# Performance work log

Hardware: AMD Instinct MI355X
Metric: run time of the kernel (lower is better)

Reference implementation:

```python
import jax, jax.numpy as jnp
import numpy as np

N = 50000      # nodes
E = 600000     # edges
D = 128        # embedding_dim
H = 256        # GENConv MLP hidden = 2*D (expansion=2, num_layers=2)
L = 2          # n_layers
EPS_MSG = 1e-7
EPS_NORM = 1e-5


def setup_inputs() -> dict:
    key = jax.random.key(0)
    ks = jax.random.split(key, 16)
    s = 0.05
    inp = {}
    inp["x"] = jax.random.normal(ks[0], (N, 1), jnp.float32)
    inp["edge_index"] = jax.random.randint(ks[1], (2, E), 0, N)
    inp["edge_attr"] = jax.random.normal(ks[2], (E, 1), jnp.float32)
    # encoders
    inp["Wn"] = jax.random.normal(ks[3], (1, D), jnp.float32) * s
    inp["bn_b"] = jnp.zeros((D,), jnp.float32)
    inp["We"] = jax.random.normal(ks[4], (1, D), jnp.float32) * s
    inp["be"] = jnp.zeros((D,), jnp.float32)
    # per-layer BatchNorm affine
    inp["bn_gamma"] = jnp.ones((L, D), jnp.float32)
    inp["bn_beta"] = jnp.zeros((L, D), jnp.float32)
    # per-layer GENConv params: learnable temperature t, MLP [D->H->D] with LayerNorm
    inp["t"] = jnp.ones((L,), jnp.float32)
    inp["W1"] = jax.random.normal(ks[5], (L, D, H), jnp.float32) * s
    inp["b1"] = jnp.zeros((L, H), jnp.float32)
    inp["ln_g"] = jnp.ones((L, H), jnp.float32)
    inp["ln_b"] = jnp.zeros((L, H), jnp.float32)
    inp["W2"] = jax.random.normal(ks[6], (L, H, D), jnp.float32) * s
    inp["b2"] = jnp.zeros((L, D), jnp.float32)
    return inp


def _segment_softmax(logits, seg, num):
    # per-channel softmax over edges grouped by destination node
    m = jax.ops.segment_max(logits, seg, num_segments=num)
    m = jnp.where(jnp.isfinite(m), m, 0.0)  # empty segments
    ex = jnp.exp(logits - m[seg])
    den = jax.ops.segment_sum(ex, seg, num_segments=num)
    return ex / (den[seg] + 1e-16)


def reference(x, edge_index, edge_attr, Wn, bn_b, We, be,
              bn_gamma, bn_beta, t, W1, b1, ln_g, ln_b, W2, b2):
    src, dst = edge_index[0], edge_index[1]
    h = x @ Wn + bn_b                 # [N, D] node encoder
    e = edge_attr @ We + be           # [E, D] edge encoder
    for l in range(L):
        # DeepGCNLayer 'res+': h_in -> BN -> ReLU -> conv -> + h_in
        mu = h.mean(axis=0)
        var = h.var(axis=0)
        hn = (h - mu) / jnp.sqrt(var + EPS_NORM) * bn_gamma[l] + bn_beta[l]
        hn = jax.nn.relu(hn)
        # GENConv: msg = relu(x_j + e) + eps; softmax-aggr with temperature t
        msg = jax.nn.relu(hn[src] + e) + EPS_MSG          # [E, D]
        alpha = _segment_softmax(msg * t[l], dst, N)      # [E, D]
        agg = jax.ops.segment_sum(msg * alpha, dst, num_segments=N)  # [N, D]
        out = agg + hn                                    # add root
        # GENConv MLP: Linear -> LayerNorm -> ReLU -> Linear
        z = out @ W1[l] + b1[l]
        zm = z.mean(axis=-1, keepdims=True)
        zv = z.var(axis=-1, keepdims=True)
        z = (z - zm) / jnp.sqrt(zv + EPS_NORM) * ln_g[l] + ln_b[l]
        z = jax.nn.relu(z)
        z = z @ W2[l] + b2[l]
        h = h + z                                         # res+ residual
    # DotProductPredictor over the same edge list
    return (h[src] * h[dst]).sum(axis=-1)                 # [E]
```

## Files before the change

kernel.cpp:

```cpp
#include <hip/hip_runtime.h>
#include <hip/hip_bf16.h>
#include <math.h>

#define NN 50000
#define NE 600000
#define MPAD 50048
#define DIM 128
#define HID 256
#define NB 49
#define HIST_BLOCKS ((NE + 255) / 256)
#define CAST_BLOCKS ((4 * DIM * HID) / 256)
#define EPS_MSG 1e-7f
#define EPS_NORM 1e-5f

typedef __attribute__((ext_vector_type(8))) short short8v;
typedef __attribute__((ext_vector_type(8))) unsigned short ushort8v;
typedef __attribute__((ext_vector_type(4))) float f32x4;

__device__ inline ushort f2bf(float f) {
    union { float f; unsigned u; } v; v.f = f;
    unsigned r = v.u + 0x7FFF + ((v.u >> 16) & 1);
    return (ushort)(r >> 16);
}
__device__ inline float bf2f(ushort u) {
    union { unsigned u; float f; } v; v.u = (unsigned)u << 16; return v.f;
}

__global__ __launch_bounds__(256) void k_setup(const float* __restrict__ x,
                                               const int* __restrict__ dst,
                                               const float* __restrict__ W1,
                                               const float* __restrict__ W2,
                                               float* __restrict__ xs,
                                               int* __restrict__ deg,
                                               ushort* __restrict__ W1t,
                                               ushort* __restrict__ W2t) {
    int b = blockIdx.x;
    if (b < 64) {
        int lane = threadIdx.x & 63;
        float s = 0.f, q = 0.f;
        for (int i = b * 256 + threadIdx.x; i < NN; i += 64 * 256) {
            float v = x[i];
            s += v; q += v * v;
        }
        #pragma unroll
        for (int off = 32; off >= 1; off >>= 1) {
            s += __shfl_xor(s, off, 64);
            q += __shfl_xor(q, off, 64);
        }
        if (lane == 0) { atomicAdd(&xs[0], s); atomicAdd(&xs[1], q); }
    } else if (b < 64 + HIST_BLOCKS) {
        int i = (b - 64) * 256 + threadIdx.x;
        if (i < NE) atomicAdd(&deg[dst[i]], 1);
    } else {
        const int chunk = DIM * HID;
        int i = (b - 64 - HIST_BLOCKS) * 256 + threadIdx.x;
        int w = i / chunk;
        int j = i - w * chunk;
        if (w < 2) {
            int r = j / HID, c = j - r * HID;
            W1t[(size_t)w * chunk + (size_t)c * DIM + r] = f2bf(W1[(size_t)w * chunk + j]);
        } else {
            int l = w - 2;
            int r = j / DIM, c = j - r * DIM;
            W2t[(size_t)l * chunk + (size_t)c * HID + r] = f2bf(W2[(size_t)l * chunk + j]);
        }
    }
}

__global__ void k_hn0(const float* __restrict__ x, const float* __restrict__ xs,
                      const float* __restrict__ Wn, const float* __restrict__ bnb,
                      const float* __restrict__ gamma, const float* __restrict__ beta,
                      ushort* __restrict__ hn, int total4) {
    int i = blockIdx.x * blockDim.x + threadIdx.x;
    if (i >= total4) return;
    int d4 = (i & 31) * 4;
    int n = i >> 5;
    float mx = xs[0] * (1.f / NN);
    float vx = xs[1] * (1.f / NN) - mx * mx;
    float xv = x[n];
    float4 w = *(const float4*)(Wn + d4);
    float4 b = *(const float4*)(bnb + d4);
    float4 g = *(const float4*)(gamma + d4);
    float4 bt = *(const float4*)(beta + d4);
    ushort4 o;
    {
        float mu = fmaf(mx, w.x, b.x), sc = rsqrtf(vx * w.x * w.x + EPS_NORM) * g.x;
        o.x = f2bf(fmaxf(fmaf(fmaf(xv, w.x, b.x) - mu, sc, bt.x), 0.f));
    }
    {
        float mu = fmaf(mx, w.y, b.y), sc = rsqrtf(vx * w.y * w.y + EPS_NORM) * g.y;
        o.y = f2bf(fmaxf(fmaf(fmaf(xv, w.y, b.y) - mu, sc, bt.y), 0.f));
    }
    {
        float mu = fmaf(mx, w.z, b.z), sc = rsqrtf(vx * w.z * w.z + EPS_NORM) * g.z;
        o.z = f2bf(fmaxf(fmaf(fmaf(xv, w.z, b.z) - mu, sc, bt.z), 0.f));
    }
    {
        float mu = fmaf(mx, w.w, b.w), sc = rsqrtf(vx * w.w * w.w + EPS_NORM) * g.w;
        o.w = f2bf(fmaxf(fmaf(fmaf(xv, w.w, b.w) - mu, sc, bt.w), 0.f));
    }
    *(ushort4*)(hn + (size_t)n * DIM + d4) = o;
}

__global__ __launch_bounds__(256) void k_scanA(const int* __restrict__ deg,
                                               int* __restrict__ partials, int n) {
    __shared__ int ws[4];
    int b = blockIdx.x;
    int t = threadIdx.x;
    int s = 0;
    #pragma unroll
    for (int i = 0; i < 4; ++i) {
        int idx = b * 1024 + t + i * 256;
        s += (idx < n) ? deg[idx] : 0;
    }
    #pragma unroll
    for (int off = 32; off >= 1; off >>= 1) s += __shfl_xor(s, off, 64);
    if ((t & 63) == 0) ws[t >> 6] = s;
    __syncthreads();
    if (t == 0) partials[b] = ws[0] + ws[1] + ws[2] + ws[3];
}

__global__ __launch_bounds__(64) void k_scanB(const int* __restrict__ partials,
                                              int* __restrict__ base,
                                              int* __restrict__ row_off) {
    int t = threadIdx.x;
    int v = (t < NB) ? partials[t] : 0;
    int x = v;
    #pragma unroll
    for (int off = 1; off < 64; off <<= 1) {
        int y = __shfl_up(x, off, 64);
        if (t >= off) x += y;
    }
    if (t < NB) base[t] = x - v;
    if (t == 0) row_off[NN] = NE;
}

__global__ __launch_bounds__(1024) void k_scanC(const int* __restrict__ deg,
                                                const int* __restrict__ base,
                                                int* __restrict__ row_off,
                                                int* __restrict__ cursor, int n) {
    __shared__ int wsum[16];
    int i = blockIdx.x * 1024 + threadIdx.x;
    int lane = threadIdx.x & 63;
    int wid = threadIdx.x >> 6;
    int v = (i < n) ? deg[i] : 0;
    int x = v;
    #pragma unroll
    for (int off = 1; off < 64; off <<= 1) {
        int y = __shfl_up(x, off, 64);
        if (lane >= off) x += y;
    }
    if (lane == 63) wsum[wid] = x;
    __syncthreads();
    if (wid == 0 && lane < 16) {
        int w = wsum[lane];
        #pragma unroll
        for (int off = 1; off < 16; off <<= 1) {
            int y = __shfl_up(w, off, 64);
            if (lane >= off) w += y;
        }
        wsum[lane] = w;
    }
    __syncthreads();
    int prev = (wid == 0) ? 0 : wsum[wid - 1];
    int excl = base[blockIdx.x] + prev + (x - v);
    if (i < n) { row_off[i] = excl; cursor[i] = excl; }
}

__global__ void k_scatter(const int* __restrict__ src, const int* __restrict__ dst,
                          const float* __restrict__ eattr, int* __restrict__ cursor,
                          int4* __restrict__ erec, int E) {
    int i = blockIdx.x * blockDim.x + threadIdx.x;
    if (i >= E) return;
    int d = dst[i];
    int pos = atomicAdd(&cursor[d], 1);
    erec[pos] = make_int4(src[i], i, __float_as_int(eattr[i]), 0);
}

__global__ void k_bn_relu(const float* __restrict__ h, const float* __restrict__ stats,
                          const float* __restrict__ gamma, const float* __restrict__ beta,
                          ushort* __restrict__ hn, int total4) {
    int i = blockIdx.x * blockDim.x + threadIdx.x;
    if (i >= total4) return;
    int d4 = (i & 31) * 4;
    int n = i >> 5;
    float4 v = *(const float4*)(h + (size_t)n * DIM + d4);
    float4 s = *(const float4*)(stats + d4);
    float4 q = *(const float4*)(stats + DIM + d4);
    float4 g = *(const float4*)(gamma + d4);
    float4 bt = *(const float4*)(beta + d4);
    ushort4 o;
    {
        float mu = s.x * (1.f / NN), var = q.x * (1.f / NN) - mu * mu;
        float sc = rsqrtf(var + EPS_NORM) * g.x;
        o.x = f2bf(fmaxf(fmaf(v.x - mu, sc, bt.x), 0.f));
    }
    {
        float mu = s.y * (1.f / NN), var = q.y * (1.f / NN) - mu * mu;
        float sc = rsqrtf(var + EPS_NORM) * g.y;
        o.y = f2bf(fmaxf(fmaf(v.y - mu, sc, bt.y), 0.f));
    }
    {
        float mu = s.z * (1.f / NN), var = q.z * (1.f / NN) - mu * mu;
        float sc = rsqrtf(var + EPS_NORM) * g.z;
        o.z = f2bf(fmaxf(fmaf(v.z - mu, sc, bt.z), 0.f));
    }
    {
        float mu = s.w * (1.f / NN), var = q.w * (1.f / NN) - mu * mu;
        float sc = rsqrtf(var + EPS_NORM) * g.w;
        o.w = f2bf(fmaxf(fmaf(v.w - mu, sc, bt.w), 0.f));
    }
    *(ushort4*)(hn + (size_t)n * DIM + d4) = o;
}

__global__ __launch_bounds__(256) void k_agg(const ushort* __restrict__ hn,
                                             const int4* __restrict__ erec,
                                             const int* __restrict__ row_off,
                                             const float* __restrict__ We,
                                             const float* __restrict__ be,
                                             const float* __restrict__ t_all, int l,
                                             ushort* __restrict__ ob, int N) {
    int n = blockIdx.x * 4 + (threadIdx.x >> 6);
    if (n >= N) return;
    int lane = threadIdx.x & 63;
    int d0 = lane * 2;
    float2 we = *(const float2*)(We + d0);
    float2 bd = *(const float2*)(be + d0);
    float t = t_all[l];
    int p0 = row_off[n], p1 = row_off[n + 1];
    int deg = p1 - p0;

    int mp = p0 + lane;
    int s_l = 0; float ea_l = 0.f;
    if (mp < p1) {
        int4 r = erec[mp];
        s_l = r.x; ea_l = __int_as_float(r.z);
    }

    float den0 = 0.f, num0 = 0.f, den1 = 0.f, num1 = 0.f;
    int kmax = deg < 64 ? deg : 64;
    int k = 0;
    for (; k + 4 <= kmax; k += 4) {
        int sA = __shfl(s_l, k, 64), sB = __shfl(s_l, k + 1, 64);
        int sC = __shfl(s_l, k + 2, 64), sD = __shfl(s_l, k + 3, 64);
        float eA = __shfl(ea_l, k, 64), eB = __shfl(ea_l, k + 1, 64);
        float eC = __shfl(ea_l, k + 2, 64), eD = __shfl(ea_l, k + 3, 64);
        uint hA = *(const uint*)(hn + (size_t)sA * DIM + d0);
        uint hB = *(const uint*)(hn + (size_t)sB * DIM + d0);
        uint hC = *(const uint*)(hn + (size_t)sC * DIM + d0);
        uint hD = *(const uint*)(hn + (size_t)sD * DIM + d0);
        {
            float m0 = fmaxf(bf2f((ushort)hA) + fmaf(eA, we.x, bd.x), 0.f) + EPS_MSG;
            float m1 = fmaxf(bf2f((ushort)(hA >> 16)) + fmaf(eA, we.y, bd.y), 0.f) + EPS_MSG;
            float x0 = __expf(m0 * t), x1 = __expf(m1 * t);
            den0 += x0; num0 += m0 * x0; den1 += x1; num1 += m1 * x1;
        }
        {
            float m0 = fmaxf(bf2f((ushort)hB) + fmaf(eB, we.x, bd.x), 0.f) + EPS_MSG;
            float m1 = fmaxf(bf2f((ushort)(hB >> 16)) + fmaf(eB, we.y, bd.y), 0.f) + EPS_MSG;
            float x0 = __expf(m0 * t), x1 = __expf(m1 * t);
            den0 += x0; num0 += m0 * x0; den1 += x1; num1 += m1 * x1;
        }
        {
            float m0 = fmaxf(bf2f((ushort)hC) + fmaf(eC, we.x, bd.x), 0.f) + EPS_MSG;
            float m1 = fmaxf(bf2f((ushort)(hC >> 16)) + fmaf(eC, we.y, bd.y), 0.f) + EPS_MSG;
            float x0 = __expf(m0 * t), x1 = __expf(m1 * t);
            den0 += x0; num0 += m0 * x0; den1 += x1; num1 += m1 * x1;
        }
        {
            float m0 = fmaxf(bf2f((ushort)hD) + fmaf(eD, we.x, bd.x), 0.f) + EPS_MSG;
            float m1 = fmaxf(bf2f((ushort)(hD >> 16)) + fmaf(eD, we.y, bd.y), 0.f) + EPS_MSG;
            float x0 = __expf(m0 * t), x1 = __expf(m1 * t);
            den0 += x0; num0 += m0 * x0; den1 += x1; num1 += m1 * x1;
        }
    }
    for (; k < kmax; ++k) {
        int s = __shfl(s_l, k, 64);
        float ea = __shfl(ea_l, k, 64);
        uint hv = *(const uint*)(hn + (size_t)s * DIM + d0);
        float m0 = fmaxf(bf2f((ushort)hv) + fmaf(ea, we.x, bd.x), 0.f) + EPS_MSG;
        float m1 = fmaxf(bf2f((ushort)(hv >> 16)) + fmaf(ea, we.y, bd.y), 0.f) + EPS_MSG;
        float x0 = __expf(m0 * t), x1 = __expf(m1 * t);
        den0 += x0; num0 += m0 * x0; den1 += x1; num1 += m1 * x1;
    }
    for (int p = p0 + 64; p < p1; ++p) {
        int4 r = erec[p];
        int s = r.x;
        float ea = __int_as_float(r.z);
        uint hv = *(const uint*)(hn + (size_t)s * DIM + d0);
        float m0 = fmaxf(bf2f((ushort)hv) + fmaf(ea, we.x, bd.x), 0.f) + EPS_MSG;
        float m1 = fmaxf(bf2f((ushort)(hv >> 16)) + fmaf(ea, we.y, bd.y), 0.f) + EPS_MSG;
        float x0 = __expf(m0 * t), x1 = __expf(m1 * t);
        den0 += x0; num0 += m0 * x0; den1 += x1; num1 += m1 * x1;
    }
    uint hr = *(const uint*)(hn + (size_t)n * DIM + d0);
    float a0 = (deg > 0) ? num0 / (den0 + 1e-16f) : 0.f;
    float a1 = (deg > 0) ? num1 / (den1 + 1e-16f) : 0.f;
    uint o = (uint)f2bf(a0 + bf2f((ushort)hr)) |
             ((uint)f2bf(a1 + bf2f((ushort)(hr >> 16))) << 16);
    *(uint*)(ob + (size_t)n * DIM + d0) = o;
}

template <int FIRST>
__global__ __launch_bounds__(256) void k_mlp(const ushort* __restrict__ A,
                                             const ushort* __restrict__ B1t,
                                             const float* __restrict__ b1,
                                             const float* __restrict__ g,
                                             const float* __restrict__ bv,
                                             const ushort* __restrict__ B2t,
                                             const float* __restrict__ b2,
                                             const float* __restrict__ x,
                                             const float* __restrict__ Wn,
                                             const float* __restrict__ bnb,
                                             float* __restrict__ C,
                                             ushort* __restrict__ hb,
                                             float* __restrict__ stats) {
    constexpr int LDZ = 264;
    __shared__ ushort Zs[32 * LDZ];
    __shared__ float red_s[4][32];
    __shared__ float red_q[4][32];
    __shared__ float murs[2][32];
    const int tid = threadIdx.x;
    const int lane = tid & 63;
    const int wid = tid >> 6;
    const int row0 = blockIdx.x * 32;
    const int wc = wid * 64;
    const int l15 = lane & 15;
    const int lq = lane >> 4;

    f32x4 acc[2][4] = {};
    #pragma unroll
    for (int ks = 0; ks < 4; ++ks) {
        int kk = ks * 32 + lq * 8;
        short8v bfr[4], afr[2];
        #pragma unroll
        for (int f = 0; f < 4; ++f)
            bfr[f] = *(const short8v*)(B1t + (size_t)(wc + f * 16 + l15) * DIM + kk);
        #pragma unroll
        for (int f = 0; f < 2; ++f)
            afr[f] = *(const short8v*)(A + (size_t)(row0 + f * 16 + l15) * DIM + kk);
        #pragma unroll
        for (int mi = 0; mi < 2; ++mi)
            #pragma unroll
            for (int ni = 0; ni < 4; ++ni)
                acc[mi][ni] = __builtin_amdgcn_mfma_f32_16x16x32_bf16(
                    afr[mi], bfr[ni], acc[mi][ni], 0, 0, 0);
    }

    float bb[4], gg[4], bb2[4];
    #pragma unroll
    for (int ni = 0; ni < 4; ++ni) {
        int col = wc + ni * 16 + l15;
        bb[ni] = b1[col]; gg[ni] = g[col]; bb2[ni] = bv[col];
    }
    #pragma unroll
    for (int mi = 0; mi < 2; ++mi) {
        #pragma unroll
        for (int j = 0; j < 4; ++j) {
            float s = 0.f, q = 0.f;
            #pragma unroll
            for (int ni = 0; ni < 4; ++ni) {
                float v = acc[mi][ni][j] + bb[ni];
                acc[mi][ni][j] = v;
                s += v; q += v * v;
            }
            #pragma unroll
            for (int off = 1; off <= 8; off <<= 1) {
                s += __shfl_xor(s, off, 64);
                q += __shfl_xor(q, off, 64);
            }
            if (l15 == 0) {
                int row = mi * 16 + lq * 4 + j;
                red_s[wid][row] = s;
                red_q[wid][row] = q;
            }
        }
    }
    __syncthreads();
    if (tid < 32) {
        float s = red_s[0][tid] + red_s[1][tid] + red_s[2][tid] + red_s[3][tid];
        float q = red_q[0][tid] + red_q[1][tid] + red_q[2][tid] + red_q[3][tid];
        float mu = s * (1.f / HID);
        float var = q * (1.f / HID) - mu * mu;
        murs[0][tid] = mu;
        murs[1][tid] = rsqrtf(var + EPS_NORM);
    }
    __syncthreads();
    #pragma unroll
    for (int mi = 0; mi < 2; ++mi) {
        #pragma unroll
        for (int j = 0; j < 4; ++j) {
            int row = mi * 16 + lq * 4 + j;
            float mu = murs[0][row], rs = murs[1][row];
            #pragma unroll
            for (int ni = 0; ni < 4; ++ni) {
                float v = fmaxf(fmaf((acc[mi][ni][j] - mu) * rs, gg[ni], bb2[ni]), 0.f);
                Zs[row * LDZ + wc + ni * 16 + l15] = f2bf(v);
            }
        }
    }
    __syncthreads();

    const int wc2 = wid * 32;
    f32x4 acc2[2][2] = {};
    #pragma unroll
    for (int ks = 0; ks < 8; ++ks) {
        int kk = ks * 32 + lq * 8;
        short8v bf2[2], af2[2];
        #pragma unroll
        for (int f = 0; f < 2; ++f)
            bf2[f] = *(const short8v*)(B2t + (size_t)(wc2 + f * 16 + l15) * HID + kk);
        #pragma unroll
        for (int f = 0; f < 2; ++f)
            af2[f] = *(const short8v*)(Zs + (f * 16 + l15) * LDZ + kk);
        #pragma unroll
        for (int mi = 0; mi < 2; ++mi)
            #pragma unroll
            for (int ni = 0; ni < 2; ++ni)
                acc2[mi][ni] = __builtin_amdgcn_mfma_f32_16x16x32_bf16(
                    af2[mi], bf2[ni], acc2[mi][ni], 0, 0, 0);
    }

    float ssum[2] = {0.f, 0.f};
    float sq[2] = {0.f, 0.f};
    #pragma unroll
    for (int ni = 0; ni < 2; ++ni) {
        int col = wc2 + ni * 16 + l15;
        float bvv = b2[col];
        float wnc = FIRST ? Wn[col] : 0.f;
        float bnc = FIRST ? bnb[col] : 0.f;
        #pragma unroll
        for (int mi = 0; mi < 2; ++mi) {
            int rowb = row0 + mi * 16 + lq * 4;
            #pragma unroll
            for (int j = 0; j < 4; ++j) {
                int gr = rowb + j;
                float base;
                if (FIRST) {
                    float xv = (gr < NN) ? x[gr] : 0.f;
                    base = fmaf(xv, wnc, bnc);
                } else {
                    base = C[(size_t)gr * DIM + col];
                }
                float v = acc2[mi][ni][j] + bvv + base;
                if (FIRST) {
                    C[(size_t)gr * DIM + col] = v;
                    bool ok = gr < NN;
                    ssum[ni] += ok ? v : 0.f;
                    sq[ni] += ok ? v * v : 0.f;
                } else {
                    hb[(size_t)gr * DIM + col] = f2bf(v);
                }
            }
        }
    }
    if (FIRST) {
        #pragma unroll
        for (int ni = 0; ni < 2; ++ni) {
            float s = ssum[ni], q = sq[ni];
            s += __shfl_xor(s, 16, 64); s += __shfl_xor(s, 32, 64);
            q += __shfl_xor(q, 16, 64); q += __shfl_xor(q, 32, 64);
            if (lq == 0) {
                int col = wc2 + ni * 16 + l15;
                atomicAdd(&stats[col], s);
                atomicAdd(&stats[DIM + col], q);
            }
        }
    }
}

__global__ __launch_bounds__(256) void k_dot(const ushort* __restrict__ hb,
                                             const int4* __restrict__ erec,
                                             const int* __restrict__ row_off,
                                             float* __restrict__ out, int N) {
    int n = blockIdx.x * 4 + (threadIdx.x >> 6);
    if (n >= N) return;
    int lane = threadIdx.x & 63;
    int sub = lane >> 4;
    int l16 = lane & 15;
    float hd[8];
    {
        ushort8v hv = *(const ushort8v*)(hb + (size_t)n * DIM + l16 * 8);
        #pragma unroll
        for (int j = 0; j < 8; ++j) hd[j] = bf2f(hv[j]);
    }
    int p0 = row_off[n], p1 = row_off[n + 1];
    int deg = p1 - p0;
    int mp = p0 + lane;
    int s_l = 0, e_l = 0;
    if (mp < p1) {
        int4 r = erec[mp];
        s_l = r.x; e_l = r.y;
    }
    int kmax = deg < 64 ? deg : 64;
    for (int k = 0; k < kmax; k += 4) {
        int idx = k + sub;
        bool ok = idx < kmax;
        int s = __shfl(s_l, idx, 64);
        int e = __shfl(e_l, idx, 64);
        ushort8v av = *(const ushort8v*)(hb + (size_t)(ok ? s : n) * DIM + l16 * 8);
        float p = 0.f;
        #pragma unroll
        for (int j = 0; j < 8; ++j) p = fmaf(bf2f(av[j]), hd[j], p);
        p += __shfl_xor(p, 1, 16);
        p += __shfl_xor(p, 2, 16);
        p += __shfl_xor(p, 4, 16);
        p += __shfl_xor(p, 8, 16);
        if (ok && l16 == 0) out[e] = p;
    }
    for (int pb = p0 + 64; pb < p1; pb += 4) {
        int pe = pb + sub;
        bool ok = pe < p1;
        int s = n, e = 0;
        if (ok) { int4 r = erec[pe]; s = r.x; e = r.y; }
        ushort8v av = *(const ushort8v*)(hb + (size_t)s * DIM + l16 * 8);
        float p = 0.f;
        #pragma unroll
        for (int j = 0; j < 8; ++j) p = fmaf(bf2f(av[j]), hd[j], p);
        p += __shfl_xor(p, 1, 16);
        p += __shfl_xor(p, 2, 16);
        p += __shfl_xor(p, 4, 16);
        p += __shfl_xor(p, 8, 16);
        if (ok && l16 == 0) out[e] = p;
    }
}

extern "C" void kernel_launch(void* const* d_in, const int* in_sizes, int n_in,
                              void* d_out, int out_size, void* d_ws, size_t ws_size,
                              hipStream_t stream) {
    const float* x        = (const float*)d_in[0];
    const int*   ei       = (const int*)d_in[1];
    const float* eattr    = (const float*)d_in[2];
    const float* Wn       = (const float*)d_in[3];
    const float* bnb      = (const float*)d_in[4];
    const float* We       = (const float*)d_in[5];
    const float* be       = (const float*)d_in[6];
    const float* bn_gamma = (const float*)d_in[7];
    const float* bn_beta  = (const float*)d_in[8];
    const float* t_all    = (const float*)d_in[9];
    const float* W1       = (const float*)d_in[10];
    const float* b1       = (const float*)d_in[11];
    const float* ln_g     = (const float*)d_in[12];
    const float* ln_b     = (const float*)d_in[13];
    const float* W2       = (const float*)d_in[14];
    const float* b2       = (const float*)d_in[15];
    float* out = (float*)d_out;

    const int N = NN, E = NE, D = DIM, H = HID;
    const int* src = ei;
    const int* dst = ei + E;

    char* ws = (char*)d_ws;
    auto alloc = [&](size_t bytes) {
        char* p = ws;
        ws += (bytes + 255) & ~(size_t)255;
        return p;
    };
    float*  h       = (float*)alloc((size_t)MPAD * D * 4);
    ushort* ob      = (ushort*)alloc((size_t)MPAD * D * 2);
    ushort* hn      = (ushort*)alloc((size_t)MPAD * D * 2);
    ushort* hb      = (ushort*)alloc((size_t)MPAD * D * 2);
    ushort* W1t     = (ushort*)alloc((size_t)2 * D * H * 2);
    ushort* W2t     = (ushort*)alloc((size_t)2 * D * H * 2);
    int4*   erec    = (int4*)alloc((size_t)E * 16);
    int*    row_off = (int*)alloc((size_t)(N + 1) * 4);
    int*    cursor  = (int*)alloc((size_t)N * 4);
    int*    deg     = (int*)alloc((size_t)N * 4);
    int*    partials= (int*)alloc((size_t)64 * 4);
    int*    pbase   = (int*)alloc((size_t)64 * 4);
    float*  stats   = (float*)alloc((size_t)2 * D * 4);
    float*  xs      = (float*)alloc((size_t)2 * 4);

    hipMemsetAsync(deg, 0, (size_t)N * 4, stream);
    hipMemsetAsync(stats, 0, 1024 + 8, stream);

    k_setup<<<64 + HIST_BLOCKS + CAST_BLOCKS, 256, 0, stream>>>(x, dst, W1, W2,
                                                                xs, deg, W1t, W2t);
    k_scanA<<<NB, 256, 0, stream>>>(deg, partials, N);
    k_scanB<<<1, 64, 0, stream>>>(partials, pbase, row_off);
    k_scanC<<<NB, 1024, 0, stream>>>(deg, pbase, row_off, cursor, N);
    k_scatter<<<(E + 255) / 256, 256, 0, stream>>>(src, dst, eattr, cursor, erec, E);
    k_hn0<<<(N * 32 + 255) / 256, 256, 0, stream>>>(x, xs, Wn, bnb, bn_gamma, bn_beta,
                                                    hn, N * 32);

    k_agg<<<(N + 3) / 4, 256, 0, stream>>>(hn, erec, row_off, We, be, t_all, 0, ob, N);
    k_mlp<1><<<MPAD / 32, 256, 0, stream>>>(ob, W1t, b1, ln_g, ln_b, W2t, b2,
                                            x, Wn, bnb, h, hb, stats);
    k_bn_relu<<<(N * 32 + 255) / 256, 256, 0, stream>>>(h, stats, bn_gamma + D, bn_beta + D,
                                                        hn, N * 32);

    k_agg<<<(N + 3) / 4, 256, 0, stream>>>(hn, erec, row_off, We, be, t_all, 1, ob, N);
    k_mlp<0><<<MPAD / 32, 256, 0, stream>>>(ob, W1t + (size_t)D * H, b1 + H,
                                            ln_g + H, ln_b + H, W2t + (size_t)D * H, b2 + D,
                                            x, Wn, bnb, h, hb, stats);

    k_dot<<<(N + 3) / 4, 256, 0, stream>>>(hb, erec, row_off, out, N);
}
```

Measured before the change: 384.0 us.

## Make MLP kernel persistent with register-resident weight fragments

The fused MLP kernel becomes persistent: a fixed grid of 512 blocks loops over 32-row tiles. Each wave loads its W1 and W2 fragments into registers once and reuses them across tiles, instead of reloading them from global memory for every tile. The A tile is loaded fully before the MFMA loop, and launch bounds request two blocks per CU. This removes repeated weight traffic but raises register pressure, about 48 short8 weight vectors per thread, which may cause spills or lower occupancy.

```diff
diff --git a/kernel.cpp b/kernel.cpp
--- a/kernel.cpp
+++ b/kernel.cpp
@@ -5,6 +5,7 @@
 #define NN 50000
 #define NE 600000
 #define MPAD 50048
+#define NT (MPAD / 32)
 #define DIM 128
 #define HID 256
 #define NB 49
@@ -302,19 +303,19 @@
 }
 
 template <int FIRST>
-__global__ __launch_bounds__(256) void k_mlp(const ushort* __restrict__ A,
-                                             const ushort* __restrict__ B1t,
-                                             const float* __restrict__ b1,
-                                             const float* __restrict__ g,
-                                             const float* __restrict__ bv,
-                                             const ushort* __restrict__ B2t,
-                                             const float* __restrict__ b2,
-                                             const float* __restrict__ x,
-                                             const float* __restrict__ Wn,
-                                             const float* __restrict__ bnb,
-                                             float* __restrict__ C,
-                                             ushort* __restrict__ hb,
-                                             float* __restrict__ stats) {
+__global__ __launch_bounds__(256, 2) void k_mlp(const ushort* __restrict__ A,
+                                                const ushort* __restrict__ B1t,
+                                                const float* __restrict__ b1,
+                                                const float* __restrict__ g,
+                                                const float* __restrict__ bv,
+                                                const ushort* __restrict__ B2t,
+                                                const float* __restrict__ b2,
+                                                const float* __restrict__ x,
+                                                const float* __restrict__ Wn,
+                                                const float* __restrict__ bnb,
+                                                float* __restrict__ C,
+                                                ushort* __restrict__ hb,
+                                                float* __restrict__ stats) {
     constexpr int LDZ = 264;
     __shared__ ushort Zs[32 * LDZ];
     __shared__ float red_s[4][32];
@@ -323,149 +324,166 @@
     const int tid = threadIdx.x;
     const int lane = tid & 63;
     const int wid = tid >> 6;
-    const int row0 = blockIdx.x * 32;
     const int wc = wid * 64;
+    const int wc2 = wid * 32;
     const int l15 = lane & 15;
     const int lq = lane >> 4;
 
-    f32x4 acc[2][4] = {};
-    #pragma unroll
-    for (int ks = 0; ks < 4; ++ks) {
-        int kk = ks * 32 + lq * 8;
-        short8v bfr[4], afr[2];
+    short8v bw1[4][4];
+    #pragma unroll
+    for (int ks = 0; ks < 4; ++ks)
         #pragma unroll
         for (int f = 0; f < 4; ++f)
-            bfr[f] = *(const short8v*)(B1t + (size_t)(wc + f * 16 + l15) * DIM + kk);
+            bw1[ks][f] = *(const short8v*)(B1t + (size_t)(wc + f * 16 + l15) * DIM +
+                                           ks * 32 + lq * 8);
+    short8v bw2[8][2];
+    #pragma unroll
+    for (int ks = 0; ks < 8; ++ks)
         #pragma unroll
         for (int f = 0; f < 2; ++f)
-            afr[f] = *(const short8v*)(A + (size_t)(row0 + f * 16 + l15) * DIM + kk);
-        #pragma unroll
-        for (int mi = 0; mi < 2; ++mi)
-            #pragma unroll
-            for (int ni = 0; ni < 4; ++ni)
-                acc[mi][ni] = __builtin_amdgcn_mfma_f32_16x16x32_bf16(
-                    afr[mi], bfr[ni], acc[mi][ni], 0, 0, 0);
-    }
-
-    float bb[4], gg[4], bb2[4];
+            bw2[ks][f] = *(const short8v*)(B2t + (size_t)(wc2 + f * 16 + l15) * HID +
+                                           ks * 32 + lq * 8);
+    float bb[4], gg[4], lb[4];
     #pragma unroll
     for (int ni = 0; ni < 4; ++ni) {
         int col = wc + ni * 16 + l15;
-        bb[ni] = b1[col]; gg[ni] = g[col]; bb2[ni] = bv[col];
-    }
-    #pragma unroll
-    for (int mi = 0; mi < 2; ++mi) {
-        #pragma unroll
-        for (int j = 0; j < 4; ++j) {
-            float s = 0.f, q = 0.f;
-            #pragma unroll
-            for (int ni = 0; ni < 4; ++ni) {
-                float v = acc[mi][ni][j] + bb[ni];
-                acc[mi][ni][j] = v;
-                s += v; q += v * v;
-            }
-            #pragma unroll
-            for (int off = 1; off <= 8; off <<= 1) {
-                s += __shfl_xor(s, off, 64);
-                q += __shfl_xor(q, off, 64);
-            }
-            if (l15 == 0) {
-                int row = mi * 16 + lq * 4 + j;
-                red_s[wid][row] = s;
-                red_q[wid][row] = q;
-            }
-        }
-    }
-    __syncthreads();
-    if (tid < 32) {
-        float s = red_s[0][tid] + red_s[1][tid] + red_s[2][tid] + red_s[3][tid];
-        float q = red_q[0][tid] + red_q[1][tid] + red_q[2][tid] + red_q[3][tid];
-        float mu = s * (1.f / HID);
-        float var = q * (1.f / HID) - mu * mu;
-        murs[0][tid] = mu;
-        murs[1][tid] = rsqrtf(var + EPS_NORM);
-    }
-    __syncthreads();
-    #pragma unroll
-    for (int mi = 0; mi < 2; ++mi) {
-        #pragma unroll
-        for (int j = 0; j < 4; ++j) {
-            int row = mi * 16 + lq * 4 + j;
-            float mu = murs[0][row], rs = murs[1][row];
-            #pragma unroll
-            for (int ni = 0; ni < 4; ++ni) {
-                float v = fmaxf(fmaf((acc[mi][ni][j] - mu) * rs, gg[ni], bb2[ni]), 0.f);
-                Zs[row * LDZ + wc + ni * 16 + l15] = f2bf(v);
-            }
-        }
-    }
-    __syncthreads();
-
-    const int wc2 = wid * 32;
-    f32x4 acc2[2][2] = {};
-    #pragma unroll
-    for (int ks = 0; ks < 8; ++ks) {
-        int kk = ks * 32 + lq * 8;
-        short8v bf2[2], af2[2];
-        #pragma unroll
-        for (int f = 0; f < 2; ++f)
-            bf2[f] = *(const short8v*)(B2t + (size_t)(wc2 + f * 16 + l15) * HID + kk);
-        #pragma unroll
-        for (int f = 0; f < 2; ++f)
-            af2[f] = *(const short8v*)(Zs + (f * 16 + l15) * LDZ + kk);
-        #pragma unroll
-        for (int mi = 0; mi < 2; ++mi)
-            #pragma unroll
-            for (int ni = 0; ni < 2; ++ni)
-                acc2[mi][ni] = __builtin_amdgcn_mfma_f32_16x16x32_bf16(
-                    af2[mi], bf2[ni], acc2[mi][ni], 0, 0, 0);
-    }
-
-    float ssum[2] = {0.f, 0.f};
-    float sq[2] = {0.f, 0.f};
+        bb[ni] = b1[col]; gg[ni] = g[col]; lb[ni] = bv[col];
+    }
+    float b2v[2], wnc[2], bnc[2];
     #pragma unroll
     for (int ni = 0; ni < 2; ++ni) {
         int col = wc2 + ni * 16 + l15;
-        float bvv = b2[col];
-        float wnc = FIRST ? Wn[col] : 0.f;
-        float bnc = FIRST ? bnb[col] : 0.f;
+        b2v[ni] = b2[col];
+        wnc[ni] = FIRST ? Wn[col] : 0.f;
+        bnc[ni] = FIRST ? bnb[col] : 0.f;
+    }
+
+    for (int tile = blockIdx.x; tile < NT; tile += gridDim.x) {
+        const int row0 = tile * 32;
+        short8v afr[4][2];
+        #pragma unroll
+        for (int ks = 0; ks < 4; ++ks)
+            #pragma unroll
+            for (int f = 0; f < 2; ++f)
+                afr[ks][f] = *(const short8v*)(A + (size_t)(row0 + f * 16 + l15) * DIM +
+                                               ks * 32 + lq * 8);
+        f32x4 acc[2][4] = {};
+        #pragma unroll
+        for (int ks = 0; ks < 4; ++ks)
+            #pragma unroll
+            for (int mi = 0; mi < 2; ++mi)
+                #pragma unroll
+                for (int ni = 0; ni < 4; ++ni)
+                    acc[mi][ni] = __builtin_amdgcn_mfma_f32_16x16x32_bf16(
+                        afr[ks][mi], bw1[ks][ni], acc[mi][ni], 0, 0, 0);
+
         #pragma unroll
         for (int mi = 0; mi < 2; ++mi) {
-            int rowb = row0 + mi * 16 + lq * 4;
             #pragma unroll
             for (int j = 0; j < 4; ++j) {
-                int gr = rowb + j;
-                float base;
-                if (FIRST) {
-                    float xv = (gr < NN) ? x[gr] : 0.f;
-                    base = fmaf(xv, wnc, bnc);
-                } else {
-                    base = C[(size_t)gr * DIM + col];
+                float s = 0.f, q = 0.f;
+                #pragma unroll
+                for (int ni = 0; ni < 4; ++ni) {
+                    float v = acc[mi][ni][j] + bb[ni];
+                    acc[mi][ni][j] = v;
+                    s += v; q += v * v;
                 }
-                float v = acc2[mi][ni][j] + bvv + base;
-                if (FIRST) {
-                    C[(size_t)gr * DIM + col] = v;
-                    bool ok = gr < NN;
-                    ssum[ni] += ok ? v : 0.f;
-                    sq[ni] += ok ? v * v : 0.f;
-                } else {
-                    hb[(size_t)gr * DIM + col] = f2bf(v);
+                #pragma unroll
+                for (int off = 1; off <= 8; off <<= 1) {
+                    s += __shfl_xor(s, off, 64);
+                    q += __shfl_xor(q, off, 64);
+                }
+                if (l15 == 0) {
+                    int row = mi * 16 + lq * 4 + j;
+                    red_s[wid][row] = s;
+                    red_q[wid][row] = q;
                 }
             }
         }
-    }
-    if (FIRST) {
+        __syncthreads();
+        if (tid < 32) {
+            float s = red_s[0][tid] + red_s[1][tid] + red_s[2][tid] + red_s[3][tid];
+            float q = red_q[0][tid] + red_q[1][tid] + red_q[2][tid] + red_q[3][tid];
+            float mu = s * (1.f / HID);
+            float var = q * (1.f / HID) - mu * mu;
+            murs[0][tid] = mu;
+            murs[1][tid] = rsqrtf(var + EPS_NORM);
+        }
+        __syncthreads();
+        #pragma unroll
+        for (int mi = 0; mi < 2; ++mi) {
+            #pragma unroll
+            for (int j = 0; j < 4; ++j) {
+                int row = mi * 16 + lq * 4 + j;
+                float mu = murs[0][row], rs = murs[1][row];
+                #pragma unroll
+                for (int ni = 0; ni < 4; ++ni) {
+                    float v = fmaxf(fmaf((acc[mi][ni][j] - mu) * rs, gg[ni], lb[ni]), 0.f);
+                    Zs[row * LDZ + wc + ni * 16 + l15] = f2bf(v);
+                }
+            }
+        }
+        __syncthreads();
+
+        f32x4 acc2[2][2] = {};
+        #pragma unroll
+        for (int ks = 0; ks < 8; ++ks) {
+            short8v af2[2];
+            #pragma unroll
+            for (int f = 0; f < 2; ++f)
+                af2[f] = *(const short8v*)(Zs + (f * 16 + l15) * LDZ + ks * 32 + lq * 8);
+            #pragma unroll
+            for (int mi = 0; mi < 2; ++mi)
+                #pragma unroll
+                for (int ni = 0; ni < 2; ++ni)
+                    acc2[mi][ni] = __builtin_amdgcn_mfma_f32_16x16x32_bf16(
+                        af2[mi], bw2[ks][ni], acc2[mi][ni], 0, 0, 0);
+        }
+
+        float ssum[2] = {0.f, 0.f};
+        float sq[2] = {0.f, 0.f};
         #pragma unroll
         for (int ni = 0; ni < 2; ++ni) {
-            float s = ssum[ni], q = sq[ni];
-            s += __shfl_xor(s, 16, 64); s += __shfl_xor(s, 32, 64);
-            q += __shfl_xor(q, 16, 64); q += __shfl_xor(q, 32, 64);
-            if (lq == 0) {
-                int col = wc2 + ni * 16 + l15;
-                atomicAdd(&stats[col], s);
-                atomicAdd(&stats[DIM + col], q);
+            int col = wc2 + ni * 16 + l15;
+            #pragma unroll
+            for (int mi = 0; mi < 2; ++mi) {
+                int rowb = row0 + mi * 16 + lq * 4;
+                #pragma unroll
+                for (int j = 0; j < 4; ++j) {
+                    int gr = rowb + j;
+                    float base;
+                    if (FIRST) {
+                        float xv = (gr < NN) ? x[gr] : 0.f;
+                        base = fmaf(xv, wnc[ni], bnc[ni]);
+                    } else {
+                        base = C[(size_t)gr * DIM + col];
+                    }
+                    float v = acc2[mi][ni][j] + b2v[ni] + base;
+                    if (FIRST) {
+                        C[(size_t)gr * DIM + col] = v;
+                        bool ok = gr < NN;
+                        ssum[ni] += ok ? v : 0.f;
+                        sq[ni] += ok ? v * v : 0.f;
+                    } else {
+                        hb[(size_t)gr * DIM + col] = f2bf(v);
+                    }
+                }
             }
         }
+        if (FIRST) {
+            #pragma unroll
+            for (int ni = 0; ni < 2; ++ni) {
+                float s = ssum[ni], q = sq[ni];
+                s += __shfl_xor(s, 16, 64); s += __shfl_xor(s, 32, 64);
+                q += __shfl_xor(q, 16, 64); q += __shfl_xor(q, 32, 64);
+                if (lq == 0) {
+                    int col = wc2 + ni * 16 + l15;
+                    atomicAdd(&stats[col], s);
+                    atomicAdd(&stats[DIM + col], q);
+                }
+            }
+        }
+        __syncthreads();
     }
 }
 
@@ -584,15 +602,15 @@
                                                     hn, N * 32);
 
     k_agg<<<(N + 3) / 4, 256, 0, stream>>>(hn, erec, row_off, We, be, t_all, 0, ob, N);
-    k_mlp<1><<<MPAD / 32, 256, 0, stream>>>(ob, W1t, b1, ln_g, ln_b, W2t, b2,
-                                            x, Wn, bnb, h, hb, stats);
+    k_mlp<1><<<512, 256, 0, stream>>>(ob, W1t, b1, ln_g, ln_b, W2t, b2,
+                                      x, Wn, bnb, h, hb, stats);
     k_bn_relu<<<(N * 32 + 255) / 256, 256, 0, stream>>>(h, stats, bn_gamma + D, bn_beta + D,
                                                         hn, N * 32);
 
     k_agg<<<(N + 3) / 4, 256, 0, stream>>>(hn, erec, row_off, We, be, t_all, 1, ob, N);
-    k_mlp<0><<<MPAD / 32, 256, 0, stream>>>(ob, W1t + (size_t)D * H, b1 + H,
-                                            ln_g + H, ln_b + H, W2t + (size_t)D * H, b2 + D,
-                                            x, Wn, bnb, h, hb, stats);
+    k_mlp<0><<<512, 256, 0, stream>>>(ob, W1t + (size_t)D * H, b1 + H,
+                                      ln_g + H, ln_b + H, W2t + (size_t)D * H, b2 + D,
+                                      x, Wn, bnb, h, hb, stats);
 
     k_dot<<<(N + 3) / 4, 256, 0, stream>>>(hb, erec, row_off, out, N);
 }
```

Measured after the change: 361.7 us. 1.06x faster.

## Split fused MLP into two per-wave GEMM kernels with separate BN stats pass

Applied to the files above, without the earlier changes.

The fused per-block MLP kernel, which kept the LayerNorm output in shared memory, is replaced by two kernels. The first computes Linear+LayerNorm+ReLU per 16-row wave and writes a bf16 Z buffer to global memory. The second reads Z back for the second GEMM. BatchNorm statistics move out of the GEMM epilogue into a dedicated reduction kernel, and the aggregation gather loop is unrolled to 8 edges so more loads are in flight. This removes block-level syncs and shared-memory traffic, at the cost of an extra round trip of roughly 25MB of Z through global memory plus extra launches and a re-read of h for the stats.

```diff
diff --git a/kernel.cpp b/kernel.cpp
--- a/kernel.cpp
+++ b/kernel.cpp
@@ -5,6 +5,7 @@
 #define NN 50000
 #define NE 600000
 #define MPAD 50048
+#define NW16 (MPAD / 16)
 #define DIM 128
 #define HID 256
 #define NB 49
@@ -177,6 +178,24 @@
     erec[pos] = make_int4(src[i], i, __float_as_int(eattr[i]), 0);
 }
 
+__global__ __launch_bounds__(256) void k_bn_stats(const float* __restrict__ h,
+                                                  float* __restrict__ stats) {
+    __shared__ float red[2][128];
+    int d = threadIdx.x & 127;
+    int rsub = threadIdx.x >> 7;
+    float s = 0.f, q = 0.f;
+    for (int r = blockIdx.x * 2 + rsub; r < NN; r += gridDim.x * 2) {
+        float v = h[(size_t)r * DIM + d];
+        s += v; q += v * v;
+    }
+    if (rsub == 0) { red[0][d] = s; red[1][d] = q; }
+    __syncthreads();
+    if (rsub == 1) {
+        atomicAdd(&stats[d], s + red[0][d]);
+        atomicAdd(&stats[DIM + d], q + red[1][d]);
+    }
+}
+
 __global__ void k_bn_relu(const float* __restrict__ h, const float* __restrict__ stats,
                           const float* __restrict__ gamma, const float* __restrict__ beta,
                           ushort* __restrict__ hn, int total4) {
@@ -240,36 +259,20 @@
     float den0 = 0.f, num0 = 0.f, den1 = 0.f, num1 = 0.f;
     int kmax = deg < 64 ? deg : 64;
     int k = 0;
-    for (; k + 4 <= kmax; k += 4) {
-        int sA = __shfl(s_l, k, 64), sB = __shfl(s_l, k + 1, 64);
-        int sC = __shfl(s_l, k + 2, 64), sD = __shfl(s_l, k + 3, 64);
-        float eA = __shfl(ea_l, k, 64), eB = __shfl(ea_l, k + 1, 64);
-        float eC = __shfl(ea_l, k + 2, 64), eD = __shfl(ea_l, k + 3, 64);
-        uint hA = *(const uint*)(hn + (size_t)sA * DIM + d0);
-        uint hB = *(const uint*)(hn + (size_t)sB * DIM + d0);
-        uint hC = *(const uint*)(hn + (size_t)sC * DIM + d0);
-        uint hD = *(const uint*)(hn + (size_t)sD * DIM + d0);
-        {
-            float m0 = fmaxf(bf2f((ushort)hA) + fmaf(eA, we.x, bd.x), 0.f) + EPS_MSG;
-            float m1 = fmaxf(bf2f((ushort)(hA >> 16)) + fmaf(eA, we.y, bd.y), 0.f) + EPS_MSG;
-            float x0 = __expf(m0 * t), x1 = __expf(m1 * t);
-            den0 += x0; num0 += m0 * x0; den1 += x1; num1 += m1 * x1;
-        }
-        {
-            float m0 = fmaxf(bf2f((ushort)hB) + fmaf(eB, we.x, bd.x), 0.f) + EPS_MSG;
-            float m1 = fmaxf(bf2f((ushort)(hB >> 16)) + fmaf(eB, we.y, bd.y), 0.f) + EPS_MSG;
-            float x0 = __expf(m0 * t), x1 = __expf(m1 * t);
-            den0 += x0; num0 += m0 * x0; den1 += x1; num1 += m1 * x1;
-        }
-        {
-            float m0 = fmaxf(bf2f((ushort)hC) + fmaf(eC, we.x, bd.x), 0.f) + EPS_MSG;
-            float m1 = fmaxf(bf2f((ushort)(hC >> 16)) + fmaf(eC, we.y, bd.y), 0.f) + EPS_MSG;
-            float x0 = __expf(m0 * t), x1 = __expf(m1 * t);
-            den0 += x0; num0 += m0 * x0; den1 += x1; num1 += m1 * x1;
-        }
-        {
-            float m0 = fmaxf(bf2f((ushort)hD) + fmaf(eD, we.x, bd.x), 0.f) + EPS_MSG;
-            float m1 = fmaxf(bf2f((ushort)(hD >> 16)) + fmaf(eD, we.y, bd.y), 0.f) + EPS_MSG;
+    for (; k + 8 <= kmax; k += 8) {
+        int ss[8]; float ee[8]; uint hv[8];
+        #pragma unroll
+        for (int u = 0; u < 8; ++u) {
+            ss[u] = __shfl(s_l, k + u, 64);
+            ee[u] = __shfl(ea_l, k + u, 64);
+        }
+        #pragma unroll
+        for (int u = 0; u < 8; ++u)
+            hv[u] = *(const uint*)(hn + (size_t)ss[u] * DIM + d0);
+        #pragma unroll
+        for (int u = 0; u < 8; ++u) {
+            float m0 = fmaxf(bf2f((ushort)hv[u]) + fmaf(ee[u], we.x, bd.x), 0.f) + EPS_MSG;
+            float m1 = fmaxf(bf2f((ushort)(hv[u] >> 16)) + fmaf(ee[u], we.y, bd.y), 0.f) + EPS_MSG;
             float x0 = __expf(m0 * t), x1 = __expf(m1 * t);
             den0 += x0; num0 += m0 * x0; den1 += x1; num1 += m1 * x1;
         }
@@ -301,170 +304,123 @@
     *(uint*)(ob + (size_t)n * DIM + d0) = o;
 }
 
-template <int FIRST>
-__global__ __launch_bounds__(256) void k_mlp(const ushort* __restrict__ A,
-                                             const ushort* __restrict__ B1t,
-                                             const float* __restrict__ b1,
-                                             const float* __restrict__ g,
-                                             const float* __restrict__ bv,
-                                             const ushort* __restrict__ B2t,
-                                             const float* __restrict__ b2,
-                                             const float* __restrict__ x,
-                                             const float* __restrict__ Wn,
-                                             const float* __restrict__ bnb,
-                                             float* __restrict__ C,
-                                             ushort* __restrict__ hb,
-                                             float* __restrict__ stats) {
-    constexpr int LDZ = 264;
-    __shared__ ushort Zs[32 * LDZ];
-    __shared__ float red_s[4][32];
-    __shared__ float red_q[4][32];
-    __shared__ float murs[2][32];
-    const int tid = threadIdx.x;
-    const int lane = tid & 63;
-    const int wid = tid >> 6;
-    const int row0 = blockIdx.x * 32;
-    const int wc = wid * 64;
-    const int l15 = lane & 15;
-    const int lq = lane >> 4;
-
-    f32x4 acc[2][4] = {};
-    #pragma unroll
-    for (int ks = 0; ks < 4; ++ks) {
-        int kk = ks * 32 + lq * 8;
-        short8v bfr[4], afr[2];
-        #pragma unroll
-        for (int f = 0; f < 4; ++f)
-            bfr[f] = *(const short8v*)(B1t + (size_t)(wc + f * 16 + l15) * DIM + kk);
-        #pragma unroll
-        for (int f = 0; f < 2; ++f)
-            afr[f] = *(const short8v*)(A + (size_t)(row0 + f * 16 + l15) * DIM + kk);
-        #pragma unroll
-        for (int mi = 0; mi < 2; ++mi)
-            #pragma unroll
-            for (int ni = 0; ni < 4; ++ni)
-                acc[mi][ni] = __builtin_amdgcn_mfma_f32_16x16x32_bf16(
-                    afr[mi], bfr[ni], acc[mi][ni], 0, 0, 0);
-    }
-
-    float bb[4], gg[4], bb2[4];
-    #pragma unroll
-    for (int ni = 0; ni < 4; ++ni) {
-        int col = wc + ni * 16 + l15;
-        bb[ni] = b1[col]; gg[ni] = g[col]; bb2[ni] = bv[col];
-    }
-    #pragma unroll
-    for (int mi = 0; mi < 2; ++mi) {
-        #pragma unroll
-        for (int j = 0; j < 4; ++j) {
-            float s = 0.f, q = 0.f;
-            #pragma unroll
-            for (int ni = 0; ni < 4; ++ni) {
-                float v = acc[mi][ni][j] + bb[ni];
-                acc[mi][ni][j] = v;
-                s += v; q += v * v;
-            }
-            #pragma unroll
-            for (int off = 1; off <= 8; off <<= 1) {
-                s += __shfl_xor(s, off, 64);
-                q += __shfl_xor(q, off, 64);
-            }
-            if (l15 == 0) {
-                int row = mi * 16 + lq * 4 + j;
-                red_s[wid][row] = s;
-                red_q[wid][row] = q;
-            }
-        }
-    }
-    __syncthreads();
-    if (tid < 32) {
-        float s = red_s[0][tid] + red_s[1][tid] + red_s[2][tid] + red_s[3][tid];
-        float q = red_q[0][tid] + red_q[1][tid] + red_q[2][tid] + red_q[3][tid];
+__global__ __launch_bounds__(256, 2) void k_g1(const ushort* __restrict__ A,
+                                               const ushort* __restrict__ B1t,
+                                               const float* __restrict__ b1,
+                                               const float* __restrict__ g,
+                                               const float* __restrict__ bv,
+                                               ushort* __restrict__ Z) {
+    int wv = (blockIdx.x * blockDim.x + threadIdx.x) >> 6;
+    int lane = threadIdx.x & 63;
+    int l15 = lane & 15, lq = lane >> 4;
+    int row0 = wv * 16;
+
+    short8v afr[4];
+    #pragma unroll
+    for (int ks = 0; ks < 4; ++ks)
+        afr[ks] = *(const short8v*)(A + (size_t)(row0 + l15) * DIM + ks * 32 + lq * 8);
+
+    float bb[16], gg[16], lb[16];
+    #pragma unroll
+    for (int nf = 0; nf < 16; ++nf) {
+        int col = nf * 16 + l15;
+        bb[nf] = b1[col]; gg[nf] = g[col]; lb[nf] = bv[col];
+    }
+
+    f32x4 acc[16] = {};
+    #pragma unroll
+    for (int nf = 0; nf < 16; ++nf) {
+        short8v bfr[4];
+        #pragma unroll
+        for (int ks = 0; ks < 4; ++ks)
+            bfr[ks] = *(const short8v*)(B1t + (size_t)(nf * 16 + l15) * DIM + ks * 32 + lq * 8);
+        #pragma unroll
+        for (int ks = 0; ks < 4; ++ks)
+            acc[nf] = __builtin_amdgcn_mfma_f32_16x16x32_bf16(afr[ks], bfr[ks], acc[nf],
+                                                              0, 0, 0);
+    }
+
+    #pragma unroll
+    for (int j = 0; j < 4; ++j) {
+        float s = 0.f, q = 0.f;
+        #pragma unroll
+        for (int nf = 0; nf < 16; ++nf) {
+            float v = acc[nf][j] + bb[nf];
+            acc[nf][j] = v;
+            s += v; q += v * v;
+        }
+        #pragma unroll
+        for (int off = 1; off <= 8; off <<= 1) {
+            s += __shfl_xor(s, off, 64);
+            q += __shfl_xor(q, off, 64);
+        }
         float mu = s * (1.f / HID);
         float var = q * (1.f / HID) - mu * mu;
-        murs[0][tid] = mu;
-        murs[1][tid] = rsqrtf(var + EPS_NORM);
-    }
-    __syncthreads();
-    #pragma unroll
-    for (int mi = 0; mi < 2; ++mi) {
-        #pragma unroll
-        for (int j = 0; j < 4; ++j) {
-            int row = mi * 16 + lq * 4 + j;
-            float mu = murs[0][row], rs = murs[1][row];
-            #pragma unroll
-            for (int ni = 0; ni < 4; ++ni) {
-                float v = fmaxf(fmaf((acc[mi][ni][j] - mu) * rs, gg[ni], bb2[ni]), 0.f);
-                Zs[row * LDZ + wc + ni * 16 + l15] = f2bf(v);
-            }
-        }
-    }
-    __syncthreads();
-
-    const int wc2 = wid * 32;
-    f32x4 acc2[2][2] = {};
-    #pragma unroll
-    for (int ks = 0; ks < 8; ++ks) {
-        int kk = ks * 32 + lq * 8;
-        short8v bf2[2], af2[2];
-        #pragma unroll
-        for (int f = 0; f < 2; ++f)
-            bf2[f] = *(const short8v*)(B2t + (size_t)(wc2 + f * 16 + l15) * HID + kk);
-        #pragma unroll
-        for (int f = 0; f < 2; ++f)
-            af2[f] = *(const short8v*)(Zs + (f * 16 + l15) * LDZ + kk);
-        #pragma unroll
-        for (int mi = 0; mi < 2; ++mi)
-            #pragma unroll
-            for (int ni = 0; ni < 2; ++ni)
-                acc2[mi][ni] = __builtin_amdgcn_mfma_f32_16x16x32_bf16(
-                    af2[mi], bf2[ni], acc2[mi][ni], 0, 0, 0);
-    }
-
-    float ssum[2] = {0.f, 0.f};
-    float sq[2] = {0.f, 0.f};
-    #pragma unroll
-    for (int ni = 0; ni < 2; ++ni) {
-        int col = wc2 + ni * 16 + l15;
-        float bvv = b2[col];
-        float wnc = FIRST ? Wn[col] : 0.f;
-        float bnc = FIRST ? bnb[col] : 0.f;
-        #pragma unroll
-        for (int mi = 0; mi < 2; ++mi) {
-            int rowb = row0 + mi * 16 + lq * 4;
-            #pragma unroll
-            for (int j = 0; j < 4; ++j) {
-                int gr = rowb + j;
-                float base;
-                if (FIRST) {
-                    float xv = (gr < NN) ? x[gr] : 0.f;
-                    base = fmaf(xv, wnc, bnc);
-                } else {
-                    base = C[(size_t)gr * DIM + col];
-                }
-                float v = acc2[mi][ni][j] + bvv + base;
-                if (FIRST) {
-                    C[(size_t)gr * DIM + col] = v;
-                    bool ok = gr < NN;
-                    ssum[ni] += ok ? v : 0.f;
-                    sq[ni] += ok ? v * v : 0.f;
-                } else {
-                    hb[(size_t)gr * DIM + col] = f2bf(v);
-                }
-            }
-        }
-    }
-    if (FIRST) {
-        #pragma unroll
-        for (int ni = 0; ni < 2; ++ni) {
-            float s = ssum[ni], q = sq[ni];
-            s += __shfl_xor(s, 16, 64); s += __shfl_xor(s, 32, 64);
-            q += __shfl_xor(q, 16, 64); q += __shfl_xor(q, 32, 64);
-            if (lq == 0) {
-                int col = wc2 + ni * 16 + l15;
-                atomicAdd(&stats[col], s);
-                atomicAdd(&stats[DIM + col], q);
-            }
+        float rs = rsqrtf(var + EPS_NORM);
+        size_t rbase = (size_t)(row0 + lq * 4 + j) * HID;
+        #pragma unroll
+        for (int nf = 0; nf < 16; ++nf) {
+            float v = fmaxf(fmaf((acc[nf][j] - mu) * rs, gg[nf], lb[nf]), 0.f);
+            Z[rbase + nf * 16 + l15] = f2bf(v);
+        }
+    }
+}
+
+template <int FIRST>
+__global__ __launch_bounds__(256, 3) void k_g2(const ushort* __restrict__ Zg,
+                                               const ushort* __restrict__ B2t,
+                                               const float* __restrict__ b2,
+                                               const float* __restrict__ x,
+                                               const float* __restrict__ Wn,
+                                               const float* __restrict__ bnb,
+                                               const float* __restrict__ Cin,
+                                               float* __restrict__ Cout,
+                                               ushort* __restrict__ hb) {
+    int wv = (blockIdx.x * blockDim.x + threadIdx.x) >> 6;
+    int lane = threadIdx.x & 63;
+    int l15 = lane & 15, lq = lane >> 4;
+    int row0 = wv * 16;
+
+    short8v af[8];
+    #pragma unroll
+    for (int ks = 0; ks < 8; ++ks)
+        af[ks] = *(const short8v*)(Zg + (size_t)(row0 + l15) * HID + ks * 32 + lq * 8);
+
+    float b2v[8], wnc[8], bnc[8];
+    #pragma unroll
+    for (int nf = 0; nf < 8; ++nf) {
+        int col = nf * 16 + l15;
+        b2v[nf] = b2[col];
+        wnc[nf] = FIRST ? Wn[col] : 0.f;
+        bnc[nf] = FIRST ? bnb[col] : 0.f;
+    }
+
+    f32x4 acc[8] = {};
+    #pragma unroll
+    for (int nf = 0; nf < 8; ++nf) {
+        short8v bfr[8];
+        #pragma unroll
+        for (int ks = 0; ks < 8; ++ks)
+            bfr[ks] = *(const short8v*)(B2t + (size_t)(nf * 16 + l15) * HID + ks * 32 + lq * 8);
+        #pragma unroll
+        for (int ks = 0; ks < 8; ++ks)
+            acc[nf] = __builtin_amdgcn_mfma_f32_16x16x32_bf16(af[ks], bfr[ks], acc[nf],
+                                                              0, 0, 0);
+    }
+
+    #pragma unroll
+    for (int j = 0; j < 4; ++j) {
+        int gr = row0 + lq * 4 + j;
+        float xb = 0.f;
+        if (FIRST) xb = (gr < NN) ? x[gr] : 0.f;
+        size_t rbase = (size_t)gr * DIM;
+        #pragma unroll
+        for (int nf = 0; nf < 8; ++nf) {
+            int col = nf * 16 + l15;
+            float base = FIRST ? fmaf(xb, wnc[nf], bnc[nf]) : Cin[rbase + col];
+            float v = acc[nf][j] + b2v[nf] + base;
+            if (FIRST) Cout[rbase + col] = v;
+            else hb[rbase + col] = f2bf(v);
         }
     }
 }
@@ -557,6 +513,7 @@
         return p;
     };
     float*  h       = (float*)alloc((size_t)MPAD * D * 4);
+    ushort* z       = (ushort*)alloc((size_t)MPAD * H * 2);
     ushort* ob      = (ushort*)alloc((size_t)MPAD * D * 2);
     ushort* hn      = (ushort*)alloc((size_t)MPAD * D * 2);
     ushort* hb      = (ushort*)alloc((size_t)MPAD * D * 2);
@@ -584,15 +541,17 @@
                                                     hn, N * 32);
 
     k_agg<<<(N + 3) / 4, 256, 0, stream>>>(hn, erec, row_off, We, be, t_all, 0, ob, N);
-    k_mlp<1><<<MPAD / 32, 256, 0, stream>>>(ob, W1t, b1, ln_g, ln_b, W2t, b2,
-                                            x, Wn, bnb, h, hb, stats);
+    k_g1<<<NW16 / 4, 256, 0, stream>>>(ob, W1t, b1, ln_g, ln_b, z);
+    k_g2<1><<<NW16 / 4, 256, 0, stream>>>(z, W2t, b2, x, Wn, bnb, h, h, hb);
+    k_bn_stats<<<256, 256, 0, stream>>>(h, stats);
     k_bn_relu<<<(N * 32 + 255) / 256, 256, 0, stream>>>(h, stats, bn_gamma + D, bn_beta + D,
                                                         hn, N * 32);
 
     k_agg<<<(N + 3) / 4, 256, 0, stream>>>(hn, erec, row_off, We, be, t_all, 1, ob, N);
-    k_mlp<0><<<MPAD / 32, 256, 0, stream>>>(ob, W1t + (size_t)D * H, b1 + H,
-                                            ln_g + H, ln_b + H, W2t + (size_t)D * H, b2 + D,
-                                            x, Wn, bnb, h, hb, stats);
+    k_g1<<<NW16 / 4, 256, 0, stream>>>(ob, W1t + (size_t)D * H, b1 + H,
+                                       ln_g + H, ln_b + H, z);
+    k_g2<0><<<NW16 / 4, 256, 0, stream>>>(z, W2t + (size_t)D * H, b2 + D,
+                                          x, Wn, bnb, h, h, hb);
 
     k_dot<<<(N + 3) / 4, 256, 0, stream>>>(hb, erec, row_off, out, N);
 }
```

Result: slower. 469.3 us (+22.2%).
